# Kernel tuning notes

Measured on AMD Instinct MI355X. Metric: run time of the kernel, lower is better.

Reference implementation:

```python
import jax, jax.numpy as jnp
import numpy as np

N = 100000
E = 1600000
IN_C, HID_C, OUT_C = 512, 128, 64
BN_EPS = 1e-5


def _add_self_loops(edge_index, n):
    loops = jnp.arange(n, dtype=edge_index.dtype)
    row = jnp.concatenate([edge_index[0], loops])
    col = jnp.concatenate([edge_index[1], loops])
    return row, col


def gcn_conv(x, W, b, row, col, n):
    # PyG GCNConv: linear first, then symmetric-normalized aggregation
    h = x @ W                                        # [N, out]
    ones = jnp.ones(row.shape[0], dtype=x.dtype)
    deg = jax.ops.segment_sum(ones, col, num_segments=n)   # in-degree incl. self-loop
    dinv = jax.lax.rsqrt(deg)                        # deg >= 1 due to self-loops
    norm = dinv[row] * dinv[col]                     # [E2]
    msg = h[row] * norm[:, None]                     # gather + scale
    out = jax.ops.segment_sum(msg, col, num_segments=n)    # scatter-add
    return out + b


def batchnorm_train(x, gamma, beta):
    mu = jnp.mean(x, axis=0)
    var = jnp.mean((x - mu) ** 2, axis=0)            # biased var, as torch BN
    return (x - mu) * jax.lax.rsqrt(var + BN_EPS) * gamma + beta


def setup_inputs() -> dict:
    key = jax.random.key(0)
    ks = jax.random.split(key, 8)
    x = jax.random.normal(ks[0], (N, IN_C), dtype=jnp.float32)
    edge_index = jax.random.randint(ks[1], (2, E), 0, N, dtype=jnp.int64)
    W1 = jax.random.normal(ks[2], (IN_C, HID_C), dtype=jnp.float32) / np.sqrt(IN_C)
    b1 = jnp.zeros((HID_C,), dtype=jnp.float32)
    gamma = jnp.ones((HID_C,), dtype=jnp.float32)
    beta = jnp.zeros((HID_C,), dtype=jnp.float32)
    W2 = jax.random.normal(ks[3], (HID_C, OUT_C), dtype=jnp.float32) / np.sqrt(HID_C)
    b2 = jnp.zeros((OUT_C,), dtype=jnp.float32)
    return {"x": x, "edge_index": edge_index, "W1": W1, "b1": b1,
            "gamma": gamma, "beta": beta, "W2": W2, "b2": b2}


def reference(x, edge_index, W1, b1, gamma, beta, W2, b2):
    row, col = _add_self_loops(edge_index, N)
    h = gcn_conv(x, W1, b1, row, col, N)
    h = batchnorm_train(h, gamma, beta)
    h = jax.nn.relu(h)
    # dropout: identity (deterministic reference)
    out = gcn_conv(h, W2, b2, row, col, N)
    return out
```

## Files before the change

kernel.cpp:

```cpp
#include <hip/hip_runtime.h>

#define NN 100000
#define NE 1600000
#define INC 512
#define HID 128
#define OUTC 64
#define BN_EPS 1e-5f

#define GS_B 1024
#define NSCB 98

#define NBLK 256
#define CHUNK (NE / NBLK)
#define BSH 8
#define NBUK ((NN + 255) >> 8)

typedef __attribute__((ext_vector_type(8))) short short8v;
typedef __attribute__((ext_vector_type(4))) float f32x4;

__device__ __forceinline__ unsigned short f2bf(float f) {
    unsigned u = __float_as_uint(f);
    u += 0x7FFFu + ((u >> 16) & 1u);
    return (unsigned short)(u >> 16);
}

__device__ __forceinline__ unsigned cvtpk(float lo, float hi) {
    unsigned r;
    asm("v_cvt_pk_bf16_f32 %0, %1, %2" : "=v"(r) : "v"(lo), "v"(hi));
    return r;
}

__device__ __forceinline__ float bflo(unsigned u) { return __uint_as_float(u << 16); }
__device__ __forceinline__ float bfhi(unsigned u) { return __uint_as_float(u & 0xFFFF0000u); }


__global__ void k_init(float* bnsum, float* bnsumsq) {
    int i = threadIdx.x;
    if (i < HID) { bnsum[i] = 0.f; bnsumsq[i] = 0.f; }
}


__global__ __launch_bounds__(256) void k_bhist(const int* __restrict__ col, int* __restrict__ bhist) {
    __shared__ int lc[NBUK];
    int tid = threadIdx.x, blk = blockIdx.x;
    for (int i = tid; i < NBUK; i += 256) lc[i] = 0;
    __syncthreads();
    int s = blk * CHUNK, e = s + CHUNK;
    for (int j = s + tid; j < e; j += 256)
        atomicAdd(&lc[col[j] >> BSH], 1);
    __syncthreads();
    for (int i = tid; i < NBUK; i += 256)
        bhist[i * NBLK + blk] = lc[i];
}

__global__ void k_gscanA(const int* __restrict__ src, int* __restrict__ dst,
                         int* __restrict__ bsum, int n) {
    __shared__ int s[GS_B];
    int tid = threadIdx.x;
    int i = blockIdx.x * GS_B + tid;
    int v = (i < n) ? src[i] : 0;
    s[tid] = v;
    __syncthreads();
    for (int off = 1; off < GS_B; off <<= 1) {
        int t = (tid >= off) ? s[tid - off] : 0;
        __syncthreads();
        s[tid] += t;
        __syncthreads();
    }
    if (i < n) dst[i] = s[tid] - v;
    if (tid == GS_B - 1) bsum[blockIdx.x] = s[tid];
}

__global__ void k_gscanB(int* bsum, int nb) {
    __shared__ int s[256];
    int tid = threadIdx.x;
    for (int i = tid; i < nb; i += blockDim.x) s[i] = bsum[i];
    __syncthreads();
    if (tid == 0) {
        int run = 0;
        for (int i = 0; i < nb; ++i) { int t = s[i]; s[i] = run; run += t; }
    }
    __syncthreads();
    for (int i = tid; i < nb; i += blockDim.x) bsum[i] = s[i];
}

__global__ __launch_bounds__(256) void k_bpart(const int* __restrict__ row, const int* __restrict__ col,
                                               const int* __restrict__ sb, const int* __restrict__ sbsum,
                                               int2* __restrict__ ebuk) {
    __shared__ int lcur[NBUK];
    int tid = threadIdx.x, blk = blockIdx.x;
    for (int i = tid; i < NBUK; i += 256) {
        int idx = i * NBLK + blk;
        lcur[i] = sb[idx] + sbsum[idx >> 10];
    }
    __syncthreads();
    int s = blk * CHUNK, e = s + CHUNK;
    for (int j = s + tid; j < e; j += 256) {
        int r = row[j], c = col[j];
        int p = atomicAdd(&lcur[c >> BSH], 1);
        ebuk[p] = make_int2(r, c);
    }
}

__global__ __launch_bounds__(256) void k_ncount(const int2* __restrict__ ebuk,
                                                const int* __restrict__ sb, const int* __restrict__ sbsum,
                                                int* __restrict__ cnt) {
    __shared__ int lc[256];
    int b = blockIdx.x, tid = threadIdx.x;
    lc[tid] = 0;
    __syncthreads();
    int i0 = b * NBLK;
    int s = sb[i0] + sbsum[i0 >> 10];
    int e2 = (b + 1 < NBUK) ? (sb[i0 + NBLK] + sbsum[(i0 + NBLK) >> 10]) : NE;
    int node0 = b << BSH;
    for (int j = s + tid; j < e2; j += 256)
        atomicAdd(&lc[ebuk[j].y - node0], 1);
    __syncthreads();
    int node = node0 + tid;
    if (node < NN) cnt[node] = lc[tid];
}

__global__ void k_scanC2(const int* __restrict__ cnt, int* __restrict__ rowptr,
                         float* __restrict__ dinv, const int* __restrict__ bsum) {
    int i = blockIdx.x * GS_B + threadIdx.x;
    if (i < NN) {
        rowptr[i] += bsum[blockIdx.x];
        dinv[i] = rsqrtf((float)(cnt[i] + 1));
    }
    if (i == 0) rowptr[NN] = NE;
}

__global__ __launch_bounds__(256) void k_bfill(const int2* __restrict__ ebuk,
                                               const int* __restrict__ sb, const int* __restrict__ sbsum,
                                               const int* __restrict__ rowptr, const float* __restrict__ dinv,
                                               int2* __restrict__ csr) {
    __shared__ int lcur[256];
    __shared__ float ld[256];
    int b = blockIdx.x, tid = threadIdx.x;
    int node0 = b << BSH;
    int node = node0 + tid;
    lcur[tid] = (node < NN) ? rowptr[node] : 0;
    ld[tid] = (node < NN) ? dinv[node] : 0.f;
    __syncthreads();
    int i0 = b * NBLK;
    int s = sb[i0] + sbsum[i0 >> 10];
    int e2 = (b + 1 < NBUK) ? (sb[i0 + NBLK] + sbsum[(i0 + NBLK) >> 10]) : NE;
    for (int j = s + tid; j < e2; j += 256) {
        int2 rc = ebuk[j];
        int li = rc.y - node0;
        float w = ld[li] * dinv[rc.x];
        int p = atomicAdd(&lcur[li], 1);
        csr[p] = make_int2(rc.x, __float_as_int(w));
    }
}


__global__ void k_prepW1(const float* __restrict__ W1, unsigned short* __restrict__ W1T) {
    int i = blockIdx.x * 256 + threadIdx.x;
    int k = i >> 7, n = i & 127;
    W1T[(size_t)n * INC + k] = f2bf(W1[i]);
}


#define G1BK 64
#define APAD 72

__global__ __launch_bounds__(256) void k_gemm1m(const float* __restrict__ x,
                                                const unsigned short* __restrict__ W1T,
                                                unsigned short* __restrict__ h1b) {
    __shared__ unsigned short As[64][APAD];
    __shared__ unsigned short Bs[128][APAD];
    int tid = threadIdx.x;
    int m0 = blockIdx.x * 64;
    int w = tid >> 6;
    int lane = tid & 63;

    f32x4 acc[4][2];
    #pragma unroll
    for (int mr = 0; mr < 4; ++mr)
        #pragma unroll
        for (int cb = 0; cb < 2; ++cb) acc[mr][cb] = (f32x4){0.f, 0.f, 0.f, 0.f};

    int ar = tid >> 2;
    int ak = (tid & 3) * 16;
    int arow = m0 + ar; if (arow >= NN) arow = NN - 1;
    const float* xr = x + (size_t)arow * INC;
    int br = tid >> 1;
    int bk = (tid & 1) * 32;
    const unsigned short* wr = W1T + (size_t)br * INC;

    int frow = lane & 15;
    int fk = (lane >> 4) * 8;

    for (int k0 = 0; k0 < INC; k0 += G1BK) {
        #pragma unroll
        for (int q = 0; q < 4; ++q) {
            float4 v = *(const float4*)(xr + k0 + ak + q * 4);
            *(uint2*)&As[ar][ak + q * 4] = make_uint2(cvtpk(v.x, v.y), cvtpk(v.z, v.w));
        }
        #pragma unroll
        for (int q = 0; q < 4; ++q) {
            *(short8v*)&Bs[br][bk + q * 8] = *(const short8v*)(wr + k0 + bk + q * 8);
        }
        __syncthreads();
        #pragma unroll
        for (int kk = 0; kk < G1BK; kk += 32) {
            short8v a[4], b[2];
            #pragma unroll
            for (int mr = 0; mr < 4; ++mr)
                a[mr] = *(const short8v*)&As[16 * mr + frow][kk + fk];
            #pragma unroll
            for (int cb = 0; cb < 2; ++cb)
                b[cb] = *(const short8v*)&Bs[32 * w + 16 * cb + frow][kk + fk];
            #pragma unroll
            for (int mr = 0; mr < 4; ++mr)
                #pragma unroll
                for (int cb = 0; cb < 2; ++cb)
                    acc[mr][cb] = __builtin_amdgcn_mfma_f32_16x16x32_bf16(b[cb], a[mr], acc[mr][cb], 0, 0, 0);
        }
        __syncthreads();
    }
    int ncol = lane & 15;
    int r4 = (lane >> 4) * 4;
    #pragma unroll
    for (int mr = 0; mr < 4; ++mr) {
        int node = m0 + 16 * mr + ncol;
        if (node < NN) {
            #pragma unroll
            for (int cb = 0; cb < 2; ++cb) {
                int ch = 32 * w + 16 * cb + r4;
                *(uint2*)&h1b[(size_t)node * HID + ch] =
                    make_uint2(cvtpk(acc[mr][cb][0], acc[mr][cb][1]),
                               cvtpk(acc[mr][cb][2], acc[mr][cb][3]));
            }
        }
    }
}


__global__ __launch_bounds__(256) void k_agg1(const unsigned short* __restrict__ h1b,
                                              const float* __restrict__ dinv,
                                              const int* __restrict__ rowptr, const int2* __restrict__ csr,
                                              const float* __restrict__ b1, unsigned* __restrict__ aggb) {
    int node = blockIdx.x * 4 + (threadIdx.x >> 6);
    int lane = threadIdx.x & 63;
    const unsigned* hp = (const unsigned*)h1b;
    size_t base = (size_t)node * 64 + lane;
    float di = dinv[node];
    unsigned hv = hp[base];
    float sx = di * di * bflo(hv);
    float sy = di * di * bfhi(hv);
    int s = rowptr[node], e = rowptr[node + 1];
    int j = s;
    for (; j + 4 <= e; j += 4) {
        int2 c0 = csr[j], c1 = csr[j + 1], c2 = csr[j + 2], c3 = csr[j + 3];
        unsigned v0 = hp[(size_t)c0.x * 64 + lane];
        unsigned v1 = hp[(size_t)c1.x * 64 + lane];
        unsigned v2 = hp[(size_t)c2.x * 64 + lane];
        unsigned v3 = hp[(size_t)c3.x * 64 + lane];
        float w0 = __int_as_float(c0.y), w1 = __int_as_float(c1.y);
        float w2 = __int_as_float(c2.y), w3 = __int_as_float(c3.y);
        sx = fmaf(w0, bflo(v0), sx); sy = fmaf(w0, bfhi(v0), sy);
        sx = fmaf(w1, bflo(v1), sx); sy = fmaf(w1, bfhi(v1), sy);
        sx = fmaf(w2, bflo(v2), sx); sy = fmaf(w2, bfhi(v2), sy);
        sx = fmaf(w3, bflo(v3), sx); sy = fmaf(w3, bfhi(v3), sy);
    }
    for (; j < e; ++j) {
        int2 c = csr[j];
        unsigned v = hp[(size_t)c.x * 64 + lane];
        float w = __int_as_float(c.y);
        sx = fmaf(w, bflo(v), sx); sy = fmaf(w, bfhi(v), sy);
    }
    float2 bb = ((const float2*)b1)[lane];
    aggb[base] = cvtpk(sx + bb.x, sy + bb.y);
}


__global__ __launch_bounds__(256) void k_bnstats(const unsigned* __restrict__ aggb,
                                                 float* __restrict__ bnsum, float* __restrict__ bnsumsq) {
    __shared__ float4 ss[256], sq[256];
    int g = threadIdx.x & 31;
    int h = threadIdx.x >> 5;
    float4 fs = make_float4(0.f, 0.f, 0.f, 0.f);
    float4 fq = make_float4(0.f, 0.f, 0.f, 0.f);
    int rows_per_block = (NN + gridDim.x - 1) / gridDim.x;
    int r0 = blockIdx.x * rows_per_block;
    int r1 = r0 + rows_per_block; if (r1 > NN) r1 = NN;
    for (int r = r0 + h; r < r1; r += 8) {
        uint2 u = *(const uint2*)(aggb + (size_t)r * 64 + 2 * g);
        float a0 = bflo(u.x), a1 = bfhi(u.x), a2 = bflo(u.y), a3 = bfhi(u.y);
        fs.x += a0; fs.y += a1; fs.z += a2; fs.w += a3;
        fq.x += a0 * a0; fq.y += a1 * a1; fq.z += a2 * a2; fq.w += a3 * a3;
    }
    ss[threadIdx.x] = fs; sq[threadIdx.x] = fq;
    __syncthreads();
    if (threadIdx.x < 32) {
        float4 as = ss[threadIdx.x], aq = sq[threadIdx.x];
        #pragma unroll
        for (int k = 1; k < 8; ++k) {
            float4 bs = ss[k * 32 + threadIdx.x], bq = sq[k * 32 + threadIdx.x];
            as.x += bs.x; as.y += bs.y; as.z += bs.z; as.w += bs.w;
            aq.x += bq.x; aq.y += bq.y; aq.z += bq.z; aq.w += bq.w;
        }
        atomicAdd(&bnsum[4 * g + 0], as.x); atomicAdd(&bnsum[4 * g + 1], as.y);
        atomicAdd(&bnsum[4 * g + 2], as.z); atomicAdd(&bnsum[4 * g + 3], as.w);
        atomicAdd(&bnsumsq[4 * g + 0], aq.x); atomicAdd(&bnsumsq[4 * g + 1], aq.y);
        atomicAdd(&bnsumsq[4 * g + 2], aq.z); atomicAdd(&bnsumsq[4 * g + 3], aq.w);
    }
}

__global__ void k_bnfinal(const float* __restrict__ bnsum, const float* __restrict__ bnsumsq,
                          const float* __restrict__ gamma, const float* __restrict__ beta,
                          float* __restrict__ bnscale, float* __restrict__ bnshift) {
    int c = threadIdx.x;
    if (c < HID) {
        float mu = bnsum[c] / (float)NN;
        float var = bnsumsq[c] / (float)NN - mu * mu;
        float sc = gamma[c] * rsqrtf(var + BN_EPS);
        bnscale[c] = sc;
        bnshift[c] = beta[c] - mu * sc;
    }
}


__global__ __launch_bounds__(256) void k_gemm2(const unsigned* __restrict__ aggb, const float* __restrict__ W2,
                                               const float* __restrict__ bnscale, const float* __restrict__ bnshift,
                                               unsigned short* __restrict__ h2b) {
    __shared__ float As2[32][66];
    __shared__ float Bs2[32][OUTC];
    int tid = threadIdx.x;
    int m0 = blockIdx.x * 64;
    int tx = tid & 15, ty = tid >> 4;
    float acc[4][4];
    #pragma unroll
    for (int r = 0; r < 4; ++r)
        #pragma unroll
        for (int c = 0; c < 4; ++c) acc[r][c] = 0.f;

    int am = tid >> 3;
    int ak = (tid & 7) * 4;
    int bk = tid >> 4;
    int bc = (tid & 15) * 4;

    for (int k0 = 0; k0 < HID; k0 += 32) {
        #pragma unroll
        for (int h = 0; h < 2; ++h) {
            int m = am + h * 32;
            int rowi = m0 + m; if (rowi >= NN) rowi = NN - 1;
            uint2 u = *(const uint2*)(aggb + (size_t)rowi * 64 + ((k0 + ak) >> 1));
            float4 sc = *(const float4*)(bnscale + k0 + ak);
            float4 sh = *(const float4*)(bnshift + k0 + ak);
            As2[ak + 0][m] = fmaxf(fmaf(bflo(u.x), sc.x, sh.x), 0.f);
            As2[ak + 1][m] = fmaxf(fmaf(bfhi(u.x), sc.y, sh.y), 0.f);
            As2[ak + 2][m] = fmaxf(fmaf(bflo(u.y), sc.z, sh.z), 0.f);
            As2[ak + 3][m] = fmaxf(fmaf(bfhi(u.y), sc.w, sh.w), 0.f);
        }
        #pragma unroll
        for (int h = 0; h < 2; ++h) {
            int k = bk + h * 16;
            *(float4*)&Bs2[k][bc] = *(const float4*)(W2 + (size_t)(k0 + k) * OUTC + bc);
        }
        __syncthreads();
        #pragma unroll
        for (int k = 0; k < 32; ++k) {
            float a[4];
            #pragma unroll
            for (int r = 0; r < 4; ++r) a[r] = As2[k][ty * 4 + r];
            float4 b = *(const float4*)&Bs2[k][tx * 4];
            #pragma unroll
            for (int r = 0; r < 4; ++r) {
                acc[r][0] = fmaf(a[r], b.x, acc[r][0]);
                acc[r][1] = fmaf(a[r], b.y, acc[r][1]);
                acc[r][2] = fmaf(a[r], b.z, acc[r][2]);
                acc[r][3] = fmaf(a[r], b.w, acc[r][3]);
            }
        }
        __syncthreads();
    }
    #pragma unroll
    for (int r = 0; r < 4; ++r) {
        int m = m0 + ty * 4 + r;
        if (m < NN) {
            *(uint2*)(h2b + (size_t)m * OUTC + tx * 4) =
                make_uint2(cvtpk(acc[r][0], acc[r][1]), cvtpk(acc[r][2], acc[r][3]));
        }
    }
}


__global__ __launch_bounds__(256) void k_agg2(const unsigned short* __restrict__ h2b,
                                              const float* __restrict__ dinv,
                                              const int* __restrict__ rowptr, const int2* __restrict__ csr,
                                              const float* __restrict__ b2, float* __restrict__ out) {
    int node = blockIdx.x * 4 + (threadIdx.x >> 6);
    int lane = threadIdx.x & 63;
    int l32 = lane & 31;
    const unsigned* hp = (const unsigned*)h2b;
    float di = dinv[node];
    float sx = 0.f, sy = 0.f;
    if (lane < 32) {
        unsigned u = hp[(size_t)node * 32 + l32];
        sx = di * di * bflo(u);
        sy = di * di * bfhi(u);
    }
    int s = rowptr[node], e = rowptr[node + 1];
    int j = s + (lane >> 5);
    for (; j + 2 < e; j += 4) {
        int2 c0 = csr[j], c1 = csr[j + 2];
        unsigned v0 = hp[(size_t)c0.x * 32 + l32];
        unsigned v1 = hp[(size_t)c1.x * 32 + l32];
        float w0 = __int_as_float(c0.y), w1 = __int_as_float(c1.y);
        sx = fmaf(w0, bflo(v0), sx); sy = fmaf(w0, bfhi(v0), sy);
        sx = fmaf(w1, bflo(v1), sx); sy = fmaf(w1, bfhi(v1), sy);
    }
    if (j < e) {
        int2 c = csr[j];
        unsigned v = hp[(size_t)c.x * 32 + l32];
        float w = __int_as_float(c.y);
        sx = fmaf(w, bflo(v), sx); sy = fmaf(w, bfhi(v), sy);
    }
    sx += __shfl_xor(sx, 32);
    sy += __shfl_xor(sy, 32);
    if (lane < 32) {
        float2 bb = ((const float2*)b2)[l32];
        ((float2*)out)[(size_t)node * 32 + l32] = make_float2(sx + bb.x, sy + bb.y);
    }
}


extern "C" void kernel_launch(void* const* d_in, const int* in_sizes, int n_in,
                              void* d_out, int out_size, void* d_ws, size_t ws_size,
                              hipStream_t stream) {
    const float* x     = (const float*)d_in[0];
    const int*   ei    = (const int*)d_in[1];
    const float* W1    = (const float*)d_in[2];
    const float* b1    = (const float*)d_in[3];
    const float* gamma = (const float*)d_in[4];
    const float* beta  = (const float*)d_in[5];
    const float* W2    = (const float*)d_in[6];
    const float* b2    = (const float*)d_in[7];
    const int* row = ei;
    const int* col = ei + NE;
    float* out = (float*)d_out;

    char* wp = (char*)d_ws;
    auto alloc = [&](size_t bytes) -> void* {
        void* p = (void*)wp;
        wp += (bytes + 255) & ~(size_t)255;
        return p;
    };
    unsigned short* h1b = (unsigned short*)alloc((size_t)NN * HID * 2);
    unsigned* aggb = (unsigned*)alloc((size_t)NN * HID * 2);
    unsigned short* h2b = (unsigned short*)alloc((size_t)NN * OUTC * 2);
    float* dinv    = (float*)alloc((size_t)NN * 4);
    float* bnsum   = (float*)alloc(HID * 4);
    float* bnsumsq = (float*)alloc(HID * 4);
    float* bnscale = (float*)alloc(HID * 4);
    float* bnshift = (float*)alloc(HID * 4);
    int*   rowptr  = (int*)alloc((size_t)(NN + 1) * 4);
    int*   cnt     = (int*)alloc((size_t)NN * 4);
    int*   bsum    = (int*)alloc(NSCB * 4);
    int*   bhist   = (int*)alloc((size_t)NBUK * NBLK * 4);
    int*   bsum2   = (int*)alloc(NSCB * 4);
    int2*  ebuk    = (int2*)alloc((size_t)NE * 8);
    int2*  csr     = (int2*)alloc((size_t)NE * 8);
    unsigned short* W1T = (unsigned short*)alloc((size_t)HID * INC * 2);

    hipLaunchKernelGGL(k_init,   dim3(1), dim3(128), 0, stream, bnsum, bnsumsq);
    hipLaunchKernelGGL(k_bhist,  dim3(NBLK), dim3(256), 0, stream, col, bhist);
    hipLaunchKernelGGL(k_gscanA, dim3(NSCB), dim3(GS_B), 0, stream, bhist, bhist, bsum2, NBUK * NBLK);
    hipLaunchKernelGGL(k_gscanB, dim3(1), dim3(128), 0, stream, bsum2, NSCB);
    hipLaunchKernelGGL(k_bpart,  dim3(NBLK), dim3(256), 0, stream, row, col, bhist, bsum2, ebuk);
    hipLaunchKernelGGL(k_ncount, dim3(NBUK), dim3(256), 0, stream, ebuk, bhist, bsum2, cnt);
    hipLaunchKernelGGL(k_gscanA, dim3(NSCB), dim3(GS_B), 0, stream, cnt, rowptr, bsum, NN);
    hipLaunchKernelGGL(k_gscanB, dim3(1), dim3(128), 0, stream, bsum, NSCB);
    hipLaunchKernelGGL(k_scanC2, dim3(NSCB), dim3(GS_B), 0, stream, cnt, rowptr, dinv, bsum);
    hipLaunchKernelGGL(k_bfill,  dim3(NBUK), dim3(256), 0, stream, ebuk, bhist, bsum2, rowptr, dinv, csr);
    hipLaunchKernelGGL(k_prepW1, dim3(256), dim3(256), 0, stream, W1, W1T);
    hipLaunchKernelGGL(k_gemm1m, dim3((NN + 63) / 64), dim3(256), 0, stream, x, W1T, h1b);
    hipLaunchKernelGGL(k_agg1,   dim3(NN / 4), dim3(256), 0, stream, h1b, dinv, rowptr, csr, b1, aggb);
    hipLaunchKernelGGL(k_bnstats, dim3(256), dim3(256), 0, stream, aggb, bnsum, bnsumsq);
    hipLaunchKernelGGL(k_bnfinal, dim3(1), dim3(128), 0, stream, bnsum, bnsumsq, gamma, beta, bnscale, bnshift);
    hipLaunchKernelGGL(k_gemm2,  dim3((NN + 63) / 64), dim3(256), 0, stream, aggb, W2, bnscale, bnshift, h2b);
    hipLaunchKernelGGL(k_agg2,   dim3(NN / 4), dim3(256), 0, stream, h2b, dinv, rowptr, csr, b2, out);
}
```

Measured before the change: 346.9 us.

## Pack CSR edges into 32-bit words and fuse degree count with local scan

Edge bucket entries and CSR entries are compressed from 8-byte int2 to 4-byte words: the bucket stores the source row plus the low 8 bits of the destination, and the CSR stores the row in 17 bits plus the source in-degree in the upper bits. Edge weights are recomputed in the aggregation kernels with rsqrt from the two degrees, so no float weight array is needed. Degree counting and the row-pointer scan are fused into a per-bucket kernel, which removes the global scan passes and the init kernel. Separately, the first GEMM gains register prefetching of the next K tile. The packing relies on N fitting in 17 bits and degree in 15 bits, and it adds rsqrt work to the gather loops in exchange for halving index traffic.

```diff
diff --git a/kernel.cpp b/kernel.cpp
--- a/kernel.cpp
+++ b/kernel.cpp
@@ -34,15 +34,11 @@
 __device__ __forceinline__ float bfhi(unsigned u) { return __uint_as_float(u & 0xFFFF0000u); }
 
 
-__global__ void k_init(float* bnsum, float* bnsumsq) {
-    int i = threadIdx.x;
-    if (i < HID) { bnsum[i] = 0.f; bnsumsq[i] = 0.f; }
-}
-
-
-__global__ __launch_bounds__(256) void k_bhist(const int* __restrict__ col, int* __restrict__ bhist) {
+__global__ __launch_bounds__(256) void k_bhist(const int* __restrict__ col, int* __restrict__ bhist,
+                                               float* bnsum, float* bnsumsq) {
     __shared__ int lc[NBUK];
     int tid = threadIdx.x, blk = blockIdx.x;
+    if (blk == 0 && tid < HID) { bnsum[tid] = 0.f; bnsumsq[tid] = 0.f; }
     for (int i = tid; i < NBUK; i += 256) lc[i] = 0;
     __syncthreads();
     int s = blk * CHUNK, e = s + CHUNK;
@@ -86,7 +82,7 @@
 
 __global__ __launch_bounds__(256) void k_bpart(const int* __restrict__ row, const int* __restrict__ col,
                                                const int* __restrict__ sb, const int* __restrict__ sbsum,
-                                               int2* __restrict__ ebuk) {
+                                               unsigned* __restrict__ ebuk) {
     __shared__ int lcur[NBUK];
     int tid = threadIdx.x, blk = blockIdx.x;
     for (int i = tid; i < NBUK; i += 256) {
@@ -98,59 +94,60 @@
     for (int j = s + tid; j < e; j += 256) {
         int r = row[j], c = col[j];
         int p = atomicAdd(&lcur[c >> BSH], 1);
-        ebuk[p] = make_int2(r, c);
-    }
-}
-
-__global__ __launch_bounds__(256) void k_ncount(const int2* __restrict__ ebuk,
-                                                const int* __restrict__ sb, const int* __restrict__ sbsum,
-                                                int* __restrict__ cnt) {
+        ebuk[p] = (unsigned)r | ((unsigned)(c & 255) << 24);
+    }
+}
+
+__global__ __launch_bounds__(256) void k_nprep(const unsigned* __restrict__ ebuk,
+                                               const int* __restrict__ sb, const int* __restrict__ sbsum,
+                                               int* __restrict__ deg, int* __restrict__ rowptr) {
     __shared__ int lc[256];
+    __shared__ int sc[256];
     int b = blockIdx.x, tid = threadIdx.x;
     lc[tid] = 0;
     __syncthreads();
     int i0 = b * NBLK;
     int s = sb[i0] + sbsum[i0 >> 10];
     int e2 = (b + 1 < NBUK) ? (sb[i0 + NBLK] + sbsum[(i0 + NBLK) >> 10]) : NE;
-    int node0 = b << BSH;
     for (int j = s + tid; j < e2; j += 256)
-        atomicAdd(&lc[ebuk[j].y - node0], 1);
-    __syncthreads();
-    int node = node0 + tid;
-    if (node < NN) cnt[node] = lc[tid];
-}
-
-__global__ void k_scanC2(const int* __restrict__ cnt, int* __restrict__ rowptr,
-                         float* __restrict__ dinv, const int* __restrict__ bsum) {
-    int i = blockIdx.x * GS_B + threadIdx.x;
-    if (i < NN) {
-        rowptr[i] += bsum[blockIdx.x];
-        dinv[i] = rsqrtf((float)(cnt[i] + 1));
-    }
-    if (i == 0) rowptr[NN] = NE;
-}
-
-__global__ __launch_bounds__(256) void k_bfill(const int2* __restrict__ ebuk,
+        atomicAdd(&lc[ebuk[j] >> 24], 1);
+    __syncthreads();
+    int v = lc[tid];
+    sc[tid] = v;
+    __syncthreads();
+    for (int off = 1; off < 256; off <<= 1) {
+        int t = (tid >= off) ? sc[tid - off] : 0;
+        __syncthreads();
+        sc[tid] += t;
+        __syncthreads();
+    }
+    int node = (b << BSH) + tid;
+    if (node < NN) {
+        deg[node] = v;
+        rowptr[node] = s + sc[tid] - v;
+    }
+    if (b == NBUK - 1 && tid == 0) rowptr[NN] = NE;
+}
+
+__global__ __launch_bounds__(256) void k_bfill(const unsigned* __restrict__ ebuk,
                                                const int* __restrict__ sb, const int* __restrict__ sbsum,
-                                               const int* __restrict__ rowptr, const float* __restrict__ dinv,
-                                               int2* __restrict__ csr) {
+                                               const int* __restrict__ rowptr, const int* __restrict__ deg,
+                                               unsigned* __restrict__ csr) {
     __shared__ int lcur[256];
-    __shared__ float ld[256];
     int b = blockIdx.x, tid = threadIdx.x;
     int node0 = b << BSH;
     int node = node0 + tid;
     lcur[tid] = (node < NN) ? rowptr[node] : 0;
-    ld[tid] = (node < NN) ? dinv[node] : 0.f;
     __syncthreads();
     int i0 = b * NBLK;
     int s = sb[i0] + sbsum[i0 >> 10];
     int e2 = (b + 1 < NBUK) ? (sb[i0 + NBLK] + sbsum[(i0 + NBLK) >> 10]) : NE;
     for (int j = s + tid; j < e2; j += 256) {
-        int2 rc = ebuk[j];
-        int li = rc.y - node0;
-        float w = ld[li] * dinv[rc.x];
+        unsigned rc = ebuk[j];
+        int li = rc >> 24;
+        int r = rc & 0xFFFFFF;
         int p = atomicAdd(&lcur[li], 1);
-        csr[p] = make_int2(rc.x, __float_as_int(w));
+        csr[p] = (unsigned)r | ((unsigned)deg[r] << 17);
     }
 }
 
@@ -192,17 +189,27 @@
     int frow = lane & 15;
     int fk = (lane >> 4) * 8;
 
+    float4 pv[4];
+    short8v pb[4];
+    #pragma unroll
+    for (int q = 0; q < 4; ++q) pv[q] = *(const float4*)(xr + ak + q * 4);
+    #pragma unroll
+    for (int q = 0; q < 4; ++q) pb[q] = *(const short8v*)(wr + bk + q * 8);
+
     for (int k0 = 0; k0 < INC; k0 += G1BK) {
         #pragma unroll
-        for (int q = 0; q < 4; ++q) {
-            float4 v = *(const float4*)(xr + k0 + ak + q * 4);
-            *(uint2*)&As[ar][ak + q * 4] = make_uint2(cvtpk(v.x, v.y), cvtpk(v.z, v.w));
-        }
-        #pragma unroll
-        for (int q = 0; q < 4; ++q) {
-            *(short8v*)&Bs[br][bk + q * 8] = *(const short8v*)(wr + k0 + bk + q * 8);
-        }
-        __syncthreads();
+        for (int q = 0; q < 4; ++q)
+            *(uint2*)&As[ar][ak + q * 4] = make_uint2(cvtpk(pv[q].x, pv[q].y), cvtpk(pv[q].z, pv[q].w));
+        #pragma unroll
+        for (int q = 0; q < 4; ++q)
+            *(short8v*)&Bs[br][bk + q * 8] = pb[q];
+        __syncthreads();
+        if (k0 + G1BK < INC) {
+            #pragma unroll
+            for (int q = 0; q < 4; ++q) pv[q] = *(const float4*)(xr + k0 + G1BK + ak + q * 4);
+            #pragma unroll
+            for (int q = 0; q < 4; ++q) pb[q] = *(const short8v*)(wr + k0 + G1BK + bk + q * 8);
+        }
         #pragma unroll
         for (int kk = 0; kk < G1BK; kk += 32) {
             short8v a[4], b[2];
@@ -239,37 +246,43 @@
 
 
 __global__ __launch_bounds__(256) void k_agg1(const unsigned short* __restrict__ h1b,
-                                              const float* __restrict__ dinv,
-                                              const int* __restrict__ rowptr, const int2* __restrict__ csr,
+                                              const int* __restrict__ deg,
+                                              const int* __restrict__ rowptr, const unsigned* __restrict__ csr,
                                               const float* __restrict__ b1, unsigned* __restrict__ aggb) {
     int node = blockIdx.x * 4 + (threadIdx.x >> 6);
     int lane = threadIdx.x & 63;
     const unsigned* hp = (const unsigned*)h1b;
     size_t base = (size_t)node * 64 + lane;
-    float di = dinv[node];
+    float dnf = (float)(deg[node] + 1);
+    float di = rsqrtf(dnf);
+    float wself = di * di;
     unsigned hv = hp[base];
-    float sx = di * di * bflo(hv);
-    float sy = di * di * bfhi(hv);
+    float sx = wself * bflo(hv);
+    float sy = wself * bfhi(hv);
     int s = rowptr[node], e = rowptr[node + 1];
     int j = s;
     for (; j + 4 <= e; j += 4) {
-        int2 c0 = csr[j], c1 = csr[j + 1], c2 = csr[j + 2], c3 = csr[j + 3];
-        unsigned v0 = hp[(size_t)c0.x * 64 + lane];
-        unsigned v1 = hp[(size_t)c1.x * 64 + lane];
-        unsigned v2 = hp[(size_t)c2.x * 64 + lane];
-        unsigned v3 = hp[(size_t)c3.x * 64 + lane];
-        float w0 = __int_as_float(c0.y), w1 = __int_as_float(c1.y);
-        float w2 = __int_as_float(c2.y), w3 = __int_as_float(c3.y);
+        unsigned c0 = csr[j], c1 = csr[j + 1], c2 = csr[j + 2], c3 = csr[j + 3];
+        int r0 = c0 & 0x1FFFF, r1 = c1 & 0x1FFFF, r2 = c2 & 0x1FFFF, r3 = c3 & 0x1FFFF;
+        unsigned v0 = hp[(size_t)r0 * 64 + lane];
+        unsigned v1 = hp[(size_t)r1 * 64 + lane];
+        unsigned v2 = hp[(size_t)r2 * 64 + lane];
+        unsigned v3 = hp[(size_t)r3 * 64 + lane];
+        float w0 = rsqrtf(dnf * (float)((c0 >> 17) + 1));
+        float w1 = rsqrtf(dnf * (float)((c1 >> 17) + 1));
+        float w2 = rsqrtf(dnf * (float)((c2 >> 17) + 1));
+        float w3 = rsqrtf(dnf * (float)((c3 >> 17) + 1));
         sx = fmaf(w0, bflo(v0), sx); sy = fmaf(w0, bfhi(v0), sy);
         sx = fmaf(w1, bflo(v1), sx); sy = fmaf(w1, bfhi(v1), sy);
         sx = fmaf(w2, bflo(v2), sx); sy = fmaf(w2, bfhi(v2), sy);
         sx = fmaf(w3, bflo(v3), sx); sy = fmaf(w3, bfhi(v3), sy);
     }
     for (; j < e; ++j) {
-        int2 c = csr[j];
-        unsigned v = hp[(size_t)c.x * 64 + lane];
-        float w = __int_as_float(c.y);
-        sx = fmaf(w, bflo(v), sx); sy = fmaf(w, bfhi(v), sy);
+        unsigned c = csr[j];
+        int r = c & 0x1FFFF;
+        unsigned v = hp[(size_t)r * 64 + lane];
+        float ww = rsqrtf(dnf * (float)((c >> 17) + 1));
+        sx = fmaf(ww, bflo(v), sx); sy = fmaf(ww, bfhi(v), sy);
     }
     float2 bb = ((const float2*)b1)[lane];
     aggb[base] = cvtpk(sx + bb.x, sy + bb.y);
@@ -389,35 +402,40 @@
 
 
 __global__ __launch_bounds__(256) void k_agg2(const unsigned short* __restrict__ h2b,
-                                              const float* __restrict__ dinv,
-                                              const int* __restrict__ rowptr, const int2* __restrict__ csr,
+                                              const int* __restrict__ deg,
+                                              const int* __restrict__ rowptr, const unsigned* __restrict__ csr,
                                               const float* __restrict__ b2, float* __restrict__ out) {
     int node = blockIdx.x * 4 + (threadIdx.x >> 6);
     int lane = threadIdx.x & 63;
     int l32 = lane & 31;
     const unsigned* hp = (const unsigned*)h2b;
-    float di = dinv[node];
+    float dnf = (float)(deg[node] + 1);
+    float di = rsqrtf(dnf);
+    float wself = di * di;
     float sx = 0.f, sy = 0.f;
     if (lane < 32) {
         unsigned u = hp[(size_t)node * 32 + l32];
-        sx = di * di * bflo(u);
-        sy = di * di * bfhi(u);
+        sx = wself * bflo(u);
+        sy = wself * bfhi(u);
     }
     int s = rowptr[node], e = rowptr[node + 1];
     int j = s + (lane >> 5);
     for (; j + 2 < e; j += 4) {
-        int2 c0 = csr[j], c1 = csr[j + 2];
-        unsigned v0 = hp[(size_t)c0.x * 32 + l32];
-        unsigned v1 = hp[(size_t)c1.x * 32 + l32];
-        float w0 = __int_as_float(c0.y), w1 = __int_as_float(c1.y);
+        unsigned c0 = csr[j], c1 = csr[j + 2];
+        int r0 = c0 & 0x1FFFF, r1 = c1 & 0x1FFFF;
+        unsigned v0 = hp[(size_t)r0 * 32 + l32];
+        unsigned v1 = hp[(size_t)r1 * 32 + l32];
+        float w0 = rsqrtf(dnf * (float)((c0 >> 17) + 1));
+        float w1 = rsqrtf(dnf * (float)((c1 >> 17) + 1));
         sx = fmaf(w0, bflo(v0), sx); sy = fmaf(w0, bfhi(v0), sy);
         sx = fmaf(w1, bflo(v1), sx); sy = fmaf(w1, bfhi(v1), sy);
     }
     if (j < e) {
-        int2 c = csr[j];
-        unsigned v = hp[(size_t)c.x * 32 + l32];
-        float w = __int_as_float(c.y);
-        sx = fmaf(w, bflo(v), sx); sy = fmaf(w, bfhi(v), sy);
+        unsigned c = csr[j];
+        int r = c & 0x1FFFF;
+        unsigned v = hp[(size_t)r * 32 + l32];
+        float ww = rsqrtf(dnf * (float)((c >> 17) + 1));
+        sx = fmaf(ww, bflo(v), sx); sy = fmaf(ww, bfhi(v), sy);
     }
     sx += __shfl_xor(sx, 32);
     sy += __shfl_xor(sy, 32);
@@ -452,35 +470,29 @@
     unsigned short* h1b = (unsigned short*)alloc((size_t)NN * HID * 2);
     unsigned* aggb = (unsigned*)alloc((size_t)NN * HID * 2);
     unsigned short* h2b = (unsigned short*)alloc((size_t)NN * OUTC * 2);
-    float* dinv    = (float*)alloc((size_t)NN * 4);
+    int*   deg     = (int*)alloc((size_t)NN * 4);
     float* bnsum   = (float*)alloc(HID * 4);
     float* bnsumsq = (float*)alloc(HID * 4);
     float* bnscale = (float*)alloc(HID * 4);
     float* bnshift = (float*)alloc(HID * 4);
     int*   rowptr  = (int*)alloc((size_t)(NN + 1) * 4);
-    int*   cnt     = (int*)alloc((size_t)NN * 4);
-    int*   bsum    = (int*)alloc(NSCB * 4);
     int*   bhist   = (int*)alloc((size_t)NBUK * NBLK * 4);
     int*   bsum2   = (int*)alloc(NSCB * 4);
-    int2*  ebuk    = (int2*)alloc((size_t)NE * 8);
-    int2*  csr     = (int2*)alloc((size_t)NE * 8);
+    unsigned* ebuk = (unsigned*)alloc((size_t)NE * 4);
+    unsigned* csr  = (unsigned*)alloc((size_t)NE * 4);
     unsigned short* W1T = (unsigned short*)alloc((size_t)HID * INC * 2);
 
-    hipLaunchKernelGGL(k_init,   dim3(1), dim3(128), 0, stream, bnsum, bnsumsq);
-    hipLaunchKernelGGL(k_bhist,  dim3(NBLK), dim3(256), 0, stream, col, bhist);
+    hipLaunchKernelGGL(k_bhist,  dim3(NBLK), dim3(256), 0, stream, col, bhist, bnsum, bnsumsq);
     hipLaunchKernelGGL(k_gscanA, dim3(NSCB), dim3(GS_B), 0, stream, bhist, bhist, bsum2, NBUK * NBLK);
     hipLaunchKernelGGL(k_gscanB, dim3(1), dim3(128), 0, stream, bsum2, NSCB);
     hipLaunchKernelGGL(k_bpart,  dim3(NBLK), dim3(256), 0, stream, row, col, bhist, bsum2, ebuk);
-    hipLaunchKernelGGL(k_ncount, dim3(NBUK), dim3(256), 0, stream, ebuk, bhist, bsum2, cnt);
-    hipLaunchKernelGGL(k_gscanA, dim3(NSCB), dim3(GS_B), 0, stream, cnt, rowptr, bsum, NN);
-    hipLaunchKernelGGL(k_gscanB, dim3(1), dim3(128), 0, stream, bsum, NSCB);
-    hipLaunchKernelGGL(k_scanC2, dim3(NSCB), dim3(GS_B), 0, stream, cnt, rowptr, dinv, bsum);
-    hipLaunchKernelGGL(k_bfill,  dim3(NBUK), dim3(256), 0, stream, ebuk, bhist, bsum2, rowptr, dinv, csr);
+    hipLaunchKernelGGL(k_nprep,  dim3(NBUK), dim3(256), 0, stream, ebuk, bhist, bsum2, deg, rowptr);
+    hipLaunchKernelGGL(k_bfill,  dim3(NBUK), dim3(256), 0, stream, ebuk, bhist, bsum2, rowptr, deg, csr);
     hipLaunchKernelGGL(k_prepW1, dim3(256), dim3(256), 0, stream, W1, W1T);
     hipLaunchKernelGGL(k_gemm1m, dim3((NN + 63) / 64), dim3(256), 0, stream, x, W1T, h1b);
-    hipLaunchKernelGGL(k_agg1,   dim3(NN / 4), dim3(256), 0, stream, h1b, dinv, rowptr, csr, b1, aggb);
+    hipLaunchKernelGGL(k_agg1,   dim3(NN / 4), dim3(256), 0, stream, h1b, deg, rowptr, csr, b1, aggb);
     hipLaunchKernelGGL(k_bnstats, dim3(256), dim3(256), 0, stream, aggb, bnsum, bnsumsq);
     hipLaunchKernelGGL(k_bnfinal, dim3(1), dim3(128), 0, stream, bnsum, bnsumsq, gamma, beta, bnscale, bnshift);
     hipLaunchKernelGGL(k_gemm2,  dim3((NN + 63) / 64), dim3(256), 0, stream, aggb, W2, bnscale, bnshift, h2b);
-    hipLaunchKernelGGL(k_agg2,   dim3(NN / 4), dim3(256), 0, stream, h2b, dinv, rowptr, csr, b2, out);
-}
+    hipLaunchKernelGGL(k_agg2,   dim3(NN / 4), dim3(256), 0, stream, h2b, deg, rowptr, csr, b2, out);
+}
```

Result: faster. 325.6 us (-6.1%).
